# Kernel tuning notes

Hardware: AMD Instinct MI355X
Metric: run time of the kernel (lower is better)

Reference implementation:

```python
import jax, jax.numpy as jnp
import numpy as np

N_NODES = 100_000
N_EDGES = 1_600_000
IN_FEAT = 128
N_HEADS = 8
OUT_FEAT = 16
HF = N_HEADS * OUT_FEAT  # 128
NEG_SLOPE = 0.2


def setup_inputs() -> dict:
    key = jax.random.key(0)
    k = jax.random.split(key, 9)
    x = jax.random.normal(k[0], (N_NODES, IN_FEAT), dtype=jnp.float32)
    src = jax.random.randint(k[1], (N_EDGES,), 0, N_NODES, dtype=jnp.int64)
    dst = jax.random.randint(k[2], (N_EDGES,), 0, N_NODES, dtype=jnp.int64)
    sv = 1.0 / np.sqrt(IN_FEAT)
    sa = 1.0 / np.sqrt(HF)
    Wv = jax.random.normal(k[3], (IN_FEAT, HF), dtype=jnp.float32) * sv
    bv = jnp.zeros((HF,), dtype=jnp.float32)
    Wq = jax.random.normal(k[4], (HF, N_HEADS), dtype=jnp.float32) * sa
    bq = jnp.zeros((N_HEADS,), dtype=jnp.float32)
    Wk = jax.random.normal(k[5], (HF, N_HEADS), dtype=jnp.float32) * sa
    bk = jnp.zeros((N_HEADS,), dtype=jnp.float32)
    return {"x": x, "src": src, "dst": dst, "Wv": Wv, "bv": bv,
            "Wq": Wq, "bq": bq, "Wk": Wk, "bk": bk}


def reference(x, src, dst, Wv, bv, Wq, bq, Wk, bk):
    # Dense projections (homogeneous graph: h_src == h_dst == h)
    h = x @ Wv + bv                       # [N, H*F]
    q = h @ Wq + bq                       # [N, H]  (query, attached via dst)
    k = h @ Wk + bk                       # [N, H]  (key, attached via src)
    u = h.reshape(N_NODES, N_HEADS, OUT_FEAT)  # [N, H, F]

    # Edge scores: u_add_v('k','q') -> e_ij = k[src] + q[dst], then leaky-relu
    e = k[src] + q[dst]                   # [E, H]
    coeff = jnp.where(e >= 0, e, NEG_SLOPE * e)

    # Segment softmax over incoming edges of each destination node
    seg_max = jax.ops.segment_max(coeff, dst, num_segments=N_NODES)   # [N, H]
    ex = jnp.exp(coeff - seg_max[dst])                                # [E, H]
    denom = jax.ops.segment_sum(ex, dst, num_segments=N_NODES)       # [N, H]
    attn = ex / denom[dst]                                           # [E, H]

    # Weighted message + scatter-sum aggregate
    m = u[src] * attn[:, :, None]                                    # [E, H, F]
    v = jax.ops.segment_sum(m, dst, num_segments=N_NODES)            # [N, H, F]

    return jnp.mean(v, axis=1)                                       # [N, F]
```

## Files before the change

### kernel.cpp

```cpp
#include <hip/hip_runtime.h>
#include <hip/hip_fp16.h>

#define NFEAT 128
#define NHEADS 8
#define OUTF 16
#define NPB 512
#define MAXNB 256
#define CAP 10240

typedef _Float16 half8 __attribute__((ext_vector_type(8)));
typedef float float4v __attribute__((ext_vector_type(4)));

__global__ __launch_bounds__(256) void prep_kernel(
    const float* __restrict__ Wv, const float* __restrict__ bv,
    const float* __restrict__ Wq, const float* __restrict__ bq,
    const float* __restrict__ Wk, const float* __restrict__ bk,
    float* __restrict__ Wvq, float* __restrict__ Wvk,
    float* __restrict__ bq2, float* __restrict__ bk2)
{
    const int t = threadIdx.x;
    const int idx = blockIdx.x * 256 + t;
    const int m  = idx >> 10;
    const int j  = (idx >> 3) & 127;
    const int hd = idx & 7;
    const float* w = m ? Wk : Wq;
    float acc = 0.f;
#pragma unroll 8
    for (int c = 0; c < NFEAT; c++) acc += Wv[j * NFEAT + c] * w[c * NHEADS + hd];
    if (m) Wvk[j * NHEADS + hd] = acc;
    else   Wvq[j * NHEADS + hd] = acc;

    if (blockIdx.x == 0 && t < 16) {
        int mm = t >> 3, hh = t & 7;
        const float* ww = mm ? Wk : Wq;
        float a = mm ? bk[hh] : bq[hh];
        for (int c = 0; c < NFEAT; c++) a += bv[c] * ww[c * NHEADS + hh];
        if (mm) bk2[hh] = a;
        else    bq2[hh] = a;
    }
}

__global__ __launch_bounds__(256) void gemm_h_kernel(
    const float* __restrict__ x, const float* __restrict__ Wv,
    const float* __restrict__ bv, const float* __restrict__ Wvq,
    const float* __restrict__ Wvk, const float* __restrict__ bq2,
    const float* __restrict__ bk2, __half* __restrict__ h,
    float* __restrict__ qarr, float* __restrict__ karr, int M)
{
    __shared__ _Float16 sw[144][136];
    const int t = threadIdx.x;

    for (int i = t; i < 128 * 128; i += 256) {
        int k = i >> 7, n = i & 127;
        sw[n][k] = (_Float16)Wv[i];
    }
    for (int i = t; i < 128 * 16; i += 256) {
        int k = i >> 4, o = i & 15;
        float v = (o < 8) ? Wvq[k * 8 + o] : Wvk[k * 8 + (o - 8)];
        sw[128 + o][k] = (_Float16)v;
    }
    __syncthreads();

    const int wave = t >> 6, lane = t & 63;
    const int quad = lane >> 4, l16 = lane & 15;
    const int nstrips = (M + 15) >> 4;

    float bvv[8];
#pragma unroll
    for (int tl = 0; tl < 8; tl++) bvv[tl] = bv[tl * 16 + l16];
    const float qb = (l16 < 8) ? bq2[l16] : bk2[l16 - 8];

#pragma unroll
    for (int s = 0; s < 2; s++) {
        const int strip = blockIdx.x * 8 + wave + s * 4;
        if (strip >= nstrips) break;
        const int row0 = strip * 16;
        const int xr = row0 + l16;
        const bool ok = (xr < M);
        const float* xp = x + (size_t)xr * NFEAT + quad * 8;

        half8 af[4];
#pragma unroll
        for (int kc = 0; kc < 4; kc++) {
            float4 f0 = make_float4(0.f, 0.f, 0.f, 0.f);
            float4 f1 = make_float4(0.f, 0.f, 0.f, 0.f);
            if (ok) {
                f0 = *(const float4*)(xp + kc * 32);
                f1 = *(const float4*)(xp + kc * 32 + 4);
            }
            half8 a;
            a[0] = (_Float16)f0.x; a[1] = (_Float16)f0.y;
            a[2] = (_Float16)f0.z; a[3] = (_Float16)f0.w;
            a[4] = (_Float16)f1.x; a[5] = (_Float16)f1.y;
            a[6] = (_Float16)f1.z; a[7] = (_Float16)f1.w;
            af[kc] = a;
        }

        float4v acc[9];
#pragma unroll
        for (int tl = 0; tl < 9; tl++) acc[tl] = (float4v){0.f, 0.f, 0.f, 0.f};

#pragma unroll
        for (int kc = 0; kc < 4; kc++) {
#pragma unroll
            for (int tl = 0; tl < 9; tl++) {
                half8 b = *(const half8*)&sw[tl * 16 + l16][kc * 32 + quad * 8];
                acc[tl] = __builtin_amdgcn_mfma_f32_16x16x32_f16(af[kc], b, acc[tl], 0, 0, 0);
            }
        }

#pragma unroll
        for (int r = 0; r < 4; r++) {
            int row = row0 + quad * 4 + r;
            if (row < M) {
#pragma unroll
                for (int tl = 0; tl < 8; tl++)
                    h[(size_t)row * NFEAT + tl * 16 + l16] =
                        __float2half(acc[tl][r] + bvv[tl]);
                float qv = acc[8][r] + qb;
                if (l16 < 8) qarr[(size_t)row * NHEADS + l16] = qv;
                else         karr[(size_t)row * NHEADS + (l16 - 8)] = qv;
            }
        }
    }
}

__global__ __launch_bounds__(1024) void bin_kernel(
    const int* __restrict__ src, const int* __restrict__ dst,
    int* __restrict__ tail, int2* __restrict__ bin, int E, int NB)
{
    __shared__ int lcnt[MAXNB];
    __shared__ int lbase[MAXNB];
    const int t = threadIdx.x;
    const int e0 = blockIdx.x * 4096;

    for (int i = t; i < NB; i += 1024) lcnt[i] = 0;
    __syncthreads();

    int sarr[4], dloc[4], bkt[4], rank[4];
#pragma unroll
    for (int k = 0; k < 4; k++) {
        int e = e0 + k * 1024 + t;
        bkt[k] = -1;
        if (e < E) {
            int d = dst[e];
            sarr[k] = src[e];
            bkt[k]  = d >> 9;
            dloc[k] = d & (NPB - 1);
            rank[k] = atomicAdd(&lcnt[bkt[k]], 1);
        }
    }
    __syncthreads();
    for (int i = t; i < NB; i += 1024)
        lbase[i] = lcnt[i] ? atomicAdd(&tail[i], lcnt[i]) : 0;
    __syncthreads();

#pragma unroll
    for (int k = 0; k < 4; k++) {
        if (bkt[k] >= 0) {
            int pos = lbase[bkt[k]] + rank[k];
            if (pos < CAP) bin[(size_t)bkt[k] * CAP + pos] = make_int2(sarr[k], dloc[k]);
        }
    }
}

__global__ __launch_bounds__(256) void bucket_scan_kernel(
    const int* __restrict__ tail, int* __restrict__ base, int NB)
{
    __shared__ int sd[256];
    int t = threadIdx.x;
    int v = (t < NB) ? tail[t] : 0;
    sd[t] = v; __syncthreads();
    for (int o = 1; o < 256; o <<= 1) {
        int u = (t >= o) ? sd[t - o] : 0;
        __syncthreads();
        sd[t] += u;
        __syncthreads();
    }
    if (t < NB) base[t] = sd[t] - v;
}

__global__ __launch_bounds__(1024) void bucket_build_kernel(
    const int2* __restrict__ bin, const int* __restrict__ tail,
    const int* __restrict__ base, int* __restrict__ deg, int* __restrict__ off,
    int* __restrict__ csr, int N)
{
    __shared__ int lcnt[NPB];
    __shared__ int lcur[NPB];
    __shared__ int lcsr[CAP];

    const int b = blockIdx.x;
    const int t = threadIdx.x;
    const int cnt = min(tail[b], CAP);
    const int gbase = base[b];
    const int n0 = b << 9;
    const int2* mybin = bin + (size_t)b * CAP;

    for (int i = t; i < NPB; i += 1024) lcnt[i] = 0;
    __syncthreads();

    for (int i = t; i < cnt; i += 1024) {
        int2 p = mybin[i];
        atomicAdd(&lcnt[p.y], 1);
    }
    __syncthreads();

    if (t < NPB) lcur[t] = lcnt[t];
    __syncthreads();
    for (int o = 1; o < NPB; o <<= 1) {
        int u = (t < NPB && t >= o) ? lcur[t - o] : 0;
        __syncthreads();
        if (t < NPB) lcur[t] += u;
        __syncthreads();
    }
    if (t < NPB) {
        int excl = lcur[t] - lcnt[t];
        lcur[t] = excl;
        int node = n0 + t;
        if (node < N) {
            deg[node] = lcnt[t];
            off[node] = gbase + excl;
        }
    }
    __syncthreads();

    for (int i = t; i < cnt; i += 1024) {
        int2 p = mybin[i];
        int r = atomicAdd(&lcur[p.y], 1);
        lcsr[r] = p.x;
    }
    __syncthreads();

    for (int i = t; i < cnt; i += 1024) csr[gbase + i] = lcsr[i];
}

__global__ __launch_bounds__(256) void agg_kernel(
    const int* __restrict__ csr, const int* __restrict__ off,
    const int* __restrict__ deg, const float* __restrict__ karr,
    const float* __restrict__ qarr, const __half* __restrict__ h,
    float* __restrict__ out, int nnodes)
{
    const int wave = threadIdx.x >> 6;
    const int lane = threadIdx.x & 63;
    const int d = blockIdx.x * 4 + wave;
    if (d >= nnodes) return;

    const int dg = deg[d];
    const int o0 = off[d];
    const int half = lane >> 5;
    const int sub  = lane & 31;
    const int hd   = sub >> 2;
    const int fi   = sub & 3;
    const int h8   = lane & 7;
    const float q1 = qarr[d * NHEADS + h8];
    const int psrc0 = (half << 3) + hd;
    const __half* hrow = h + (hd << 4) + (fi << 2);

    float den = 0.f, a0 = 0.f, a1 = 0.f, a2 = 0.f, a3 = 0.f;

    for (int c0 = 0; c0 < dg; c0 += 64) {
        const int cnt = min(64, dg - c0);
        int sv = (lane < cnt) ? csr[o0 + c0 + lane] : 0;
        for (int g0 = 0; g0 < cnt; g0 += 8) {
            const int epos = g0 + (lane >> 3);
            int s8 = __shfl(sv, epos, 64);
            float p8 = 0.f;
            if (epos < cnt) {
                float c = karr[s8 * NHEADS + h8] + q1;
                c = fmaxf(c, 0.2f * c);
                p8 = __expf(c);
            }
#pragma unroll
            for (int j = 0; j < 4; ++j) {
                int sl  = __shfl(sv, g0 + (j << 1) + half, 64);
                float p = __shfl(p8, psrc0 + (j << 4), 64);
                float2 raw = *(const float2*)(hrow + (size_t)sl * NFEAT);
                __half2 v01 = *(__half2*)&raw.x;
                __half2 v23 = *(__half2*)&raw.y;
                float2 f01 = __half22float2(v01);
                float2 f23 = __half22float2(v23);
                den += p;
                a0 += p * f01.x; a1 += p * f01.y;
                a2 += p * f23.x; a3 += p * f23.y;
            }
        }
    }

    den += __shfl_xor(den, 32, 64);
    a0  += __shfl_xor(a0, 32, 64);
    a1  += __shfl_xor(a1, 32, 64);
    a2  += __shfl_xor(a2, 32, 64);
    a3  += __shfl_xor(a3, 32, 64);

    if (dg > 0) {
        float inv = 0.125f / den;
        a0 *= inv; a1 *= inv; a2 *= inv; a3 *= inv;
    } else {
        a0 = a1 = a2 = a3 = 0.f;
    }
#pragma unroll
    for (int o = 4; o <= 16; o <<= 1) {
        a0 += __shfl_xor(a0, o, 64);
        a1 += __shfl_xor(a1, o, 64);
        a2 += __shfl_xor(a2, o, 64);
        a3 += __shfl_xor(a3, o, 64);
    }

    if (lane < 4) {
        float4* o4 = (float4*)(out + (size_t)d * OUTF);
        o4[lane] = make_float4(a0, a1, a2, a3);
    }
}

extern "C" void kernel_launch(void* const* d_in, const int* in_sizes, int n_in,
                              void* d_out, int out_size, void* d_ws, size_t ws_size,
                              hipStream_t stream)
{
    const float* x   = (const float*)d_in[0];
    const int*   src = (const int*)d_in[1];
    const int*   dst = (const int*)d_in[2];
    const float* Wv  = (const float*)d_in[3];
    const float* bv  = (const float*)d_in[4];
    const float* Wq  = (const float*)d_in[5];
    const float* bq  = (const float*)d_in[6];
    const float* Wk  = (const float*)d_in[7];
    const float* bk  = (const float*)d_in[8];
    float* out = (float*)d_out;

    const int N = in_sizes[0] / NFEAT;
    const int E = in_sizes[1];
    const int NB = (N + NPB - 1) / NPB;

    __half* h   = (__half*)d_ws;
    float* qarr = (float*)d_ws + (size_t)N * (NFEAT / 2);
    float* karr = qarr + (size_t)N * NHEADS;
    int* deg    = (int*)(karr + (size_t)N * NHEADS);
    int* off    = deg + N;
    int* csr    = off + N;
    float* Wvq  = (float*)(csr + E);
    float* Wvk  = Wvq + NFEAT * NHEADS;
    float* bq2  = Wvk + NFEAT * NHEADS;
    float* bk2  = bq2 + NHEADS;
    int* tail   = (int*)(bk2 + NHEADS);
    int* base   = tail + 256;
    int2* bin   = (int2*)(base + 256);

    hipMemsetAsync(tail, 0, MAXNB * sizeof(int), stream);

    prep_kernel<<<dim3(8), dim3(256), 0, stream>>>(Wv, bv, Wq, bq, Wk, bk,
                                                   Wvq, Wvk, bq2, bk2);

    bin_kernel<<<dim3((E + 4095) / 4096), dim3(1024), 0, stream>>>(
        src, dst, tail, bin, E, NB);

    bucket_scan_kernel<<<dim3(1), dim3(256), 0, stream>>>(tail, base, NB);

    bucket_build_kernel<<<dim3(NB), dim3(1024), 0, stream>>>(
        bin, tail, base, deg, off, csr, N);

    const int nstrips = (N + 15) / 16;
    gemm_h_kernel<<<dim3((nstrips + 7) / 8), dim3(256), 0, stream>>>(
        x, Wv, bv, Wvq, Wvk, bq2, bk2, h, qarr, karr, N);

    agg_kernel<<<dim3((N + 3) / 4), dim3(256), 0, stream>>>(
        csr, off, deg, karr, qarr, h, out, N);
}
```

Measured before the change: 239.7 us.

## Pack bin entries, fold bucket scan into build, half2 FMA aggregation

Shrinks buckets to 256 nodes and packs each edge's source and local destination into one 32-bit int, halving bin traffic. The separate bucket scan kernel is removed and each build block recomputes the prefix over bucket tails itself, saving one launch. The aggregation kernel now loads 16 bytes of fp16 features per lane and accumulates with packed half2 FMAs, with attention weights pre-scaled to limit fp16 overflow. In exchange, fp16 accumulation loses precision, the packed source index limits node ids to 24 bits, and CAP=4736 risks silently dropping edges when a bucket is unusually full.

Measured after the change: 237.0 us. About the same (-1.1%).

```diff
diff --git a/kernel.cpp b/kernel.cpp
--- a/kernel.cpp
+++ b/kernel.cpp
@@ -4,9 +4,9 @@
 #define NFEAT 128
 #define NHEADS 8
 #define OUTF 16
-#define NPB 512
-#define MAXNB 256
-#define CAP 10240
+#define NPB 256
+#define MAXNB 512
+#define CAP 4736
 
 typedef _Float16 half8 __attribute__((ext_vector_type(8)));
 typedef float float4v __attribute__((ext_vector_type(4)));
@@ -127,26 +127,25 @@
 
 __global__ __launch_bounds__(1024) void bin_kernel(
     const int* __restrict__ src, const int* __restrict__ dst,
-    int* __restrict__ tail, int2* __restrict__ bin, int E, int NB)
+    int* __restrict__ tail, int* __restrict__ bin, int E, int NB)
 {
     __shared__ int lcnt[MAXNB];
     __shared__ int lbase[MAXNB];
     const int t = threadIdx.x;
-    const int e0 = blockIdx.x * 4096;
+    const int e0 = blockIdx.x * 8192;
 
     for (int i = t; i < NB; i += 1024) lcnt[i] = 0;
     __syncthreads();
 
-    int sarr[4], dloc[4], bkt[4], rank[4];
-#pragma unroll
-    for (int k = 0; k < 4; k++) {
+    int pack[8], bkt[8], rank[8];
+#pragma unroll
+    for (int k = 0; k < 8; k++) {
         int e = e0 + k * 1024 + t;
         bkt[k] = -1;
         if (e < E) {
             int d = dst[e];
-            sarr[k] = src[e];
-            bkt[k]  = d >> 9;
-            dloc[k] = d & (NPB - 1);
+            pack[k] = (src[e] << 8) | (d & (NPB - 1));
+            bkt[k]  = d >> 8;
             rank[k] = atomicAdd(&lcnt[bkt[k]], 1);
         }
     }
@@ -156,53 +155,43 @@
     __syncthreads();
 
 #pragma unroll
-    for (int k = 0; k < 4; k++) {
+    for (int k = 0; k < 8; k++) {
         if (bkt[k] >= 0) {
             int pos = lbase[bkt[k]] + rank[k];
-            if (pos < CAP) bin[(size_t)bkt[k] * CAP + pos] = make_int2(sarr[k], dloc[k]);
-        }
-    }
-}
-
-__global__ __launch_bounds__(256) void bucket_scan_kernel(
-    const int* __restrict__ tail, int* __restrict__ base, int NB)
-{
-    __shared__ int sd[256];
-    int t = threadIdx.x;
-    int v = (t < NB) ? tail[t] : 0;
-    sd[t] = v; __syncthreads();
-    for (int o = 1; o < 256; o <<= 1) {
-        int u = (t >= o) ? sd[t - o] : 0;
-        __syncthreads();
-        sd[t] += u;
-        __syncthreads();
-    }
-    if (t < NB) base[t] = sd[t] - v;
+            if (pos < CAP) bin[(size_t)bkt[k] * CAP + pos] = pack[k];
+        }
+    }
 }
 
 __global__ __launch_bounds__(1024) void bucket_build_kernel(
-    const int2* __restrict__ bin, const int* __restrict__ tail,
-    const int* __restrict__ base, int* __restrict__ deg, int* __restrict__ off,
-    int* __restrict__ csr, int N)
-{
+    const int* __restrict__ bin, const int* __restrict__ tail,
+    int* __restrict__ deg, int* __restrict__ off,
+    int* __restrict__ csr, int N, int NB)
+{
+    __shared__ int stail[MAXNB];
     __shared__ int lcnt[NPB];
     __shared__ int lcur[NPB];
     __shared__ int lcsr[CAP];
 
     const int b = blockIdx.x;
     const int t = threadIdx.x;
+
+    for (int i = t; i < MAXNB; i += 1024) stail[i] = (i < NB) ? tail[i] : 0;
+    if (t < NPB) lcnt[t] = 0;
+    __syncthreads();
+
+    for (int o = 1; o < MAXNB; o <<= 1) {
+        int u = (t < MAXNB && t >= o) ? stail[t - o] : 0;
+        __syncthreads();
+        if (t < MAXNB) stail[t] += u;
+        __syncthreads();
+    }
+    const int gbase = (b > 0) ? stail[b - 1] : 0;
     const int cnt = min(tail[b], CAP);
-    const int gbase = base[b];
-    const int n0 = b << 9;
-    const int2* mybin = bin + (size_t)b * CAP;
-
-    for (int i = t; i < NPB; i += 1024) lcnt[i] = 0;
-    __syncthreads();
-
-    for (int i = t; i < cnt; i += 1024) {
-        int2 p = mybin[i];
-        atomicAdd(&lcnt[p.y], 1);
-    }
+    const int n0 = b << 8;
+    const int* mybin = bin + (size_t)b * CAP;
+
+    for (int i = t; i < cnt; i += 1024) atomicAdd(&lcnt[mybin[i] & (NPB - 1)], 1);
     __syncthreads();
 
     if (t < NPB) lcur[t] = lcnt[t];
@@ -225,9 +214,9 @@
     __syncthreads();
 
     for (int i = t; i < cnt; i += 1024) {
-        int2 p = mybin[i];
-        int r = atomicAdd(&lcur[p.y], 1);
-        lcsr[r] = p.x;
+        int p = mybin[i];
+        int r = atomicAdd(&lcur[p & (NPB - 1)], 1);
+        lcsr[r] = p >> 8;
     }
     __syncthreads();
 
@@ -247,16 +236,18 @@
 
     const int dg = deg[d];
     const int o0 = off[d];
-    const int half = lane >> 5;
-    const int sub  = lane & 31;
-    const int hd   = sub >> 2;
-    const int fi   = sub & 3;
-    const int h8   = lane & 7;
+    const int h8  = lane & 7;
+    const int eg  = lane >> 4;
+    const int l16 = lane & 15;
+    const int hd  = l16 >> 1;
     const float q1 = qarr[d * NHEADS + h8];
-    const int psrc0 = (half << 3) + hd;
-    const __half* hrow = h + (hd << 4) + (fi << 2);
-
-    float den = 0.f, a0 = 0.f, a1 = 0.f, a2 = 0.f, a3 = 0.f;
+    const __half* hbase = h + l16 * 8;
+
+    __half2 acc0 = __float2half2_rn(0.f);
+    __half2 acc1 = __float2half2_rn(0.f);
+    __half2 acc2 = __float2half2_rn(0.f);
+    __half2 acc3 = __float2half2_rn(0.f);
+    float den8 = 0.f;
 
     for (int c0 = 0; c0 < dg; c0 += 64) {
         const int cnt = min(64, dg - c0);
@@ -264,51 +255,63 @@
         for (int g0 = 0; g0 < cnt; g0 += 8) {
             const int epos = g0 + (lane >> 3);
             int s8 = __shfl(sv, epos, 64);
-            float p8 = 0.f;
+            float p = 0.f;
             if (epos < cnt) {
                 float c = karr[s8 * NHEADS + h8] + q1;
                 c = fmaxf(c, 0.2f * c);
-                p8 = __expf(c);
-            }
-#pragma unroll
-            for (int j = 0; j < 4; ++j) {
-                int sl  = __shfl(sv, g0 + (j << 1) + half, 64);
-                float p = __shfl(p8, psrc0 + (j << 4), 64);
-                float2 raw = *(const float2*)(hrow + (size_t)sl * NFEAT);
-                __half2 v01 = *(__half2*)&raw.x;
-                __half2 v23 = *(__half2*)&raw.y;
-                float2 f01 = __half22float2(v01);
-                float2 f23 = __half22float2(v23);
-                den += p;
-                a0 += p * f01.x; a1 += p * f01.y;
-                a2 += p * f23.x; a3 += p * f23.y;
-            }
-        }
-    }
-
-    den += __shfl_xor(den, 32, 64);
-    a0  += __shfl_xor(a0, 32, 64);
-    a1  += __shfl_xor(a1, 32, 64);
-    a2  += __shfl_xor(a2, 32, 64);
-    a3  += __shfl_xor(a3, 32, 64);
-
-    if (dg > 0) {
-        float inv = 0.125f / den;
-        a0 *= inv; a1 *= inv; a2 *= inv; a3 *= inv;
-    } else {
-        a0 = a1 = a2 = a3 = 0.f;
-    }
-#pragma unroll
-    for (int o = 4; o <= 16; o <<= 1) {
-        a0 += __shfl_xor(a0, o, 64);
-        a1 += __shfl_xor(a1, o, 64);
-        a2 += __shfl_xor(a2, o, 64);
-        a3 += __shfl_xor(a3, o, 64);
-    }
-
-    if (lane < 4) {
-        float4* o4 = (float4*)(out + (size_t)d * OUTF);
-        o4[lane] = make_float4(a0, a1, a2, a3);
+                p = __expf(c) * 0.0009765625f;
+            }
+            den8 += p;
+            __half2 ph2 = __half2half2(__float2half(p));
+            int phi = *(int*)&ph2;
+#pragma unroll
+            for (int i = 0; i < 2; ++i) {
+                int jr  = (i << 2) + eg;
+                int sl  = __shfl(sv, g0 + jr, 64);
+                int pw  = __shfl(phi, (jr << 3) + hd, 64);
+                __half2 pv = *(__half2*)&pw;
+                float4 raw = *(const float4*)(hbase + (size_t)sl * NFEAT);
+                __half2 v0 = *(__half2*)&raw.x;
+                __half2 v1 = *(__half2*)&raw.y;
+                __half2 v2 = *(__half2*)&raw.z;
+                __half2 v3 = *(__half2*)&raw.w;
+                acc0 = __hfma2(pv, v0, acc0);
+                acc1 = __hfma2(pv, v1, acc1);
+                acc2 = __hfma2(pv, v2, acc2);
+                acc3 = __hfma2(pv, v3, acc3);
+            }
+        }
+    }
+
+    den8 += __shfl_xor(den8, 8, 64);
+    den8 += __shfl_xor(den8, 16, 64);
+    den8 += __shfl_xor(den8, 32, 64);
+    float dh = __shfl(den8, hd, 64);
+
+    float f[8];
+    f[0] = __low2float(acc0); f[1] = __high2float(acc0);
+    f[2] = __low2float(acc1); f[3] = __high2float(acc1);
+    f[4] = __low2float(acc2); f[5] = __high2float(acc2);
+    f[6] = __low2float(acc3); f[7] = __high2float(acc3);
+
+#pragma unroll
+    for (int o = 16; o <= 32; o <<= 1)
+#pragma unroll
+        for (int i = 0; i < 8; i++) f[i] += __shfl_xor(f[i], o, 64);
+
+    const float inv = (dg > 0) ? 0.125f / dh : 0.f;
+#pragma unroll
+    for (int i = 0; i < 8; i++) f[i] *= inv;
+
+#pragma unroll
+    for (int o = 2; o <= 8; o <<= 1)
+#pragma unroll
+        for (int i = 0; i < 8; i++) f[i] += __shfl_xor(f[i], o, 64);
+
+    if (lane < 2) {
+        float4* o4 = (float4*)(out + (size_t)d * OUTF + lane * 8);
+        o4[0] = make_float4(f[0], f[1], f[2], f[3]);
+        o4[1] = make_float4(f[4], f[5], f[6], f[7]);
     }
 }
 
@@ -342,21 +345,18 @@
     float* bq2  = Wvk + NFEAT * NHEADS;
     float* bk2  = bq2 + NHEADS;
     int* tail   = (int*)(bk2 + NHEADS);
-    int* base   = tail + 256;
-    int2* bin   = (int2*)(base + 256);
+    int* bin    = tail + MAXNB;
 
     hipMemsetAsync(tail, 0, MAXNB * sizeof(int), stream);
 
     prep_kernel<<<dim3(8), dim3(256), 0, stream>>>(Wv, bv, Wq, bq, Wk, bk,
                                                    Wvq, Wvk, bq2, bk2);
 
-    bin_kernel<<<dim3((E + 4095) / 4096), dim3(1024), 0, stream>>>(
+    bin_kernel<<<dim3((E + 8191) / 8192), dim3(1024), 0, stream>>>(
         src, dst, tail, bin, E, NB);
 
-    bucket_scan_kernel<<<dim3(1), dim3(256), 0, stream>>>(tail, base, NB);
-
     bucket_build_kernel<<<dim3(NB), dim3(1024), 0, stream>>>(
-        bin, tail, base, deg, off, csr, N);
+        bin, tail, deg, off, csr, N, NB);
 
     const int nstrips = (N + 15) / 16;
     gemm_h_kernel<<<dim3((nstrips + 7) / 8), dim3(256), 0, stream>>>(
```
